# Kernel optimization log

Hardware: AMD Instinct MI355X
Metric: run time of the kernel (lower is better)

The kernel has to match this reference:

```python
import jax, jax.numpy as jnp
from jax import lax
import numpy as np

B, L, N = 128, 16, 20000
H_IN, H, H_T = 512, 1024, 128


def setup_inputs() -> dict:
    key = jax.random.key(0)
    ks = jax.random.split(key, 8)
    def xav(k, shape):
        fan_in, fan_out = shape[1], shape[0]
        a = jnp.sqrt(6.0 / (fan_in + fan_out))
        return jax.random.uniform(k, shape, jnp.float32, -a, a)
    v = jax.random.uniform(ks[0], (B, L, N), jnp.float32)
    t = jax.random.uniform(ks[1], (B, L), jnp.float32)
    W_down = xav(ks[2], (H_IN, N))
    Wt_up_w = xav(ks[3], (H_T, 1))
    Wt_up_b = jnp.zeros((H_T,), jnp.float32)
    W_vt = xav(ks[4], (H_IN, H_IN + H_T))
    k_lstm = 1.0 / jnp.sqrt(H)
    W_ih = jax.random.uniform(ks[5], (4 * H, H_IN), jnp.float32, -k_lstm, k_lstm)
    W_hh = jax.random.uniform(ks[6], (4 * H, H), jnp.float32, -k_lstm, k_lstm)
    b_ih = jnp.zeros((4 * H,), jnp.float32)
    b_hh = jnp.zeros((4 * H,), jnp.float32)
    lin_w = xav(ks[7], (1, H))
    lin_b = jnp.zeros((1,), jnp.float32)
    return {"v": v, "t": t, "W_down": W_down, "Wt_up_w": Wt_up_w,
            "Wt_up_b": Wt_up_b, "W_vt": W_vt, "W_ih": W_ih, "W_hh": W_hh,
            "b_ih": b_ih, "b_hh": b_hh, "lin_w": lin_w, "lin_b": lin_b}


def reference(v, t, W_down, Wt_up_w, Wt_up_b, W_vt, W_ih, W_hh, b_ih, b_hh, lin_w, lin_b):
    b, rw_len, n = v.shape
    h_dim = W_hh.shape[1]
    # W_down: [B,L,N] @ [N,H_in] -> [B,L,H_in]
    vd = jnp.einsum('bln,dn->bld', v, W_down)
    # Wt_up: scalar time -> [B,L,H_t]
    te = t[..., None] * Wt_up_w[:, 0] + Wt_up_b
    vt = jnp.concatenate([vd, te], axis=-1)          # [B,L,H_in+H_t]
    inputs = jnp.einsum('blk,ik->bli', vt, W_vt)     # [B,L,H_in]
    # precompute input-side LSTM gate projections for all steps
    xg = jnp.einsum('bli,gi->blg', inputs, W_ih) + b_ih  # [B,L,4H]
    xg = jnp.swapaxes(xg, 0, 1)                      # [L,B,4H] for scan

    def step(carry, xg_t):
        h, c = carry
        gates = xg_t + h @ W_hh.T + b_hh             # [B,4H]
        i, f, g, o = jnp.split(gates, 4, axis=-1)    # PyTorch gate order i,f,g,o
        i = jax.nn.sigmoid(i)
        f = jax.nn.sigmoid(f)
        g = jnp.tanh(g)
        o = jax.nn.sigmoid(o)
        c = f * c + i * g
        h = o * jnp.tanh(c)
        return (h, c), None

    h0 = jnp.zeros((b, h_dim), v.dtype)
    c0 = jnp.zeros((b, h_dim), v.dtype)
    (h, _), _ = lax.scan(step, (h0, c0), xg)
    pred = h @ lin_w.T + lin_b                       # [B,1]
    return pred
```

## Files before the change

### kernel.cpp

```cpp
#include <hip/hip_runtime.h>

typedef _Float16 f16;
typedef _Float16 f16x2 __attribute__((ext_vector_type(2)));
typedef _Float16 f16x4 __attribute__((ext_vector_type(4)));
typedef _Float16 f16x8 __attribute__((ext_vector_type(8)));
typedef float f32x4 __attribute__((ext_vector_type(4)));

__device__ __forceinline__ f32x4 mfma16(f16x8 a, f16x8 b, f32x4 c) {
  return __builtin_amdgcn_mfma_f32_16x16x32_f16(a, b, c, 0, 0, 0);
}

__device__ __forceinline__ float sigmoid_(float x) { return 1.f / (1.f + __expf(-x)); }
__device__ __forceinline__ float tanh_(float x) { return 1.f - 2.f / (__expf(2.f * x) + 1.f); }

__global__ void cvt3_kernel(const float* __restrict__ s0, f16* __restrict__ d0, int n0,
                            const float* __restrict__ s1, f16* __restrict__ d1, int n1,
                            const float* __restrict__ s2, f16* __restrict__ d2, int n2) {
  int i = blockIdx.x * 256 + threadIdx.x;
  const float* s;
  f16* d;
  int j;
  if (i < n0) {
    s = s0; d = d0; j = i;
  } else if (i < n0 + n1) {
    s = s1; d = d1; j = i - n0;
  } else if (i < n0 + n1 + n2) {
    s = s2; d = d2; j = i - n0 - n1;
  } else {
    return;
  }
  float4 v = ((const float4*)s)[j];
  f16x4 h = {(f16)v.x, (f16)v.y, (f16)v.z, (f16)v.w};
  ((f16x4*)d)[j] = h;
}

__global__ __launch_bounds__(256, 3) void gemm1_kernel(
    const float* __restrict__ A, const float* __restrict__ B, f16* __restrict__ P) {
  constexpr int K = 20000;
  __shared__ f16 Al[128][44];
  __shared__ f16 Bl[128][44];
  int tid = threadIdx.x;
  int split = blockIdx.x;
  int m0 = (blockIdx.y >> 2) * 128, n0 = (blockIdx.y & 3) * 128;
  int it0 = (split * 625) >> 4, it1 = ((split + 1) * 625) >> 4;
  int wid = tid >> 6, lane = tid & 63;
  int wm = wid & 1, wn = wid >> 1;
  int lm = lane & 15, quad = lane >> 4;
  int srow = tid >> 1, sseg = (tid & 1) * 16;

  const float* aptr = A + (size_t)(m0 + srow) * K + sseg;
  const float* bptr = B + (size_t)(n0 + srow) * K + sseg;

  float4 Ar[4], Br[4];
  {
    int k0 = it0 * 32;
#pragma unroll
    for (int j = 0; j < 4; ++j) {
      Ar[j] = *(const float4*)(aptr + k0 + j * 4);
      Br[j] = *(const float4*)(bptr + k0 + j * 4);
    }
  }

  f32x4 acc[4][4];
#pragma unroll
  for (int i = 0; i < 4; ++i)
#pragma unroll
    for (int j = 0; j < 4; ++j) acc[i][j] = (f32x4){0.f, 0.f, 0.f, 0.f};

  for (int it = it0; it < it1; ++it) {
    __syncthreads();
    {
      f16x8 pa0 = {(f16)Ar[0].x, (f16)Ar[0].y, (f16)Ar[0].z, (f16)Ar[0].w,
                   (f16)Ar[1].x, (f16)Ar[1].y, (f16)Ar[1].z, (f16)Ar[1].w};
      f16x8 pa1 = {(f16)Ar[2].x, (f16)Ar[2].y, (f16)Ar[2].z, (f16)Ar[2].w,
                   (f16)Ar[3].x, (f16)Ar[3].y, (f16)Ar[3].z, (f16)Ar[3].w};
      f16x8 pb0 = {(f16)Br[0].x, (f16)Br[0].y, (f16)Br[0].z, (f16)Br[0].w,
                   (f16)Br[1].x, (f16)Br[1].y, (f16)Br[1].z, (f16)Br[1].w};
      f16x8 pb1 = {(f16)Br[2].x, (f16)Br[2].y, (f16)Br[2].z, (f16)Br[2].w,
                   (f16)Br[3].x, (f16)Br[3].y, (f16)Br[3].z, (f16)Br[3].w};
      *(f16x8*)&Al[srow][sseg] = pa0;
      *(f16x8*)&Al[srow][sseg + 8] = pa1;
      *(f16x8*)&Bl[srow][sseg] = pb0;
      *(f16x8*)&Bl[srow][sseg + 8] = pb1;
    }
    if (it + 1 < it1) {
      int kn = (it + 1) * 32;
#pragma unroll
      for (int j = 0; j < 4; ++j) {
        Ar[j] = *(const float4*)(aptr + kn + j * 4);
        Br[j] = *(const float4*)(bptr + kn + j * 4);
      }
    }
    __syncthreads();
    f16x8 af[4];
#pragma unroll
    for (int mi = 0; mi < 4; ++mi) af[mi] = *(const f16x8*)&Al[wm * 64 + mi * 16 + lm][quad * 8];
#pragma unroll
    for (int ni = 0; ni < 4; ++ni) {
      f16x8 bf = *(const f16x8*)&Bl[wn * 64 + ni * 16 + lm][quad * 8];
#pragma unroll
      for (int mi = 0; mi < 4; ++mi) acc[mi][ni] = mfma16(af[mi], bf, acc[mi][ni]);
    }
  }
  size_t base = (size_t)split * 2048;
#pragma unroll
  for (int mi = 0; mi < 4; ++mi)
#pragma unroll
    for (int ni = 0; ni < 4; ++ni)
#pragma unroll
      for (int r = 0; r < 4; ++r) {
        int row = m0 + wm * 64 + mi * 16 + quad * 4 + r;
        int col = n0 + wn * 64 + ni * 16 + lm;
        P[(base + row) * 512 + col] = (f16)acc[mi][ni][r];
      }
}

__global__ void build_vt_kernel(const f16* __restrict__ P, const float* __restrict__ t,
                                const float* __restrict__ wtw, const float* __restrict__ wtb,
                                f16* __restrict__ vt) {
  int m = blockIdx.x;
  float tv = t[m];
  for (int c = threadIdx.x; c < 640; c += 256) {
    float val;
    if (c < 512) {
      val = 0.f;
#pragma unroll
      for (int s = 0; s < 16; ++s) val += (float)P[((size_t)s * 2048 + m) * 512 + c];
    } else {
      val = tv * wtw[c - 512] + wtb[c - 512];
    }
    vt[(size_t)m * 640 + c] = (f16)val;
  }
}

template <int TM, int TN, int EPI>
__global__ __launch_bounds__(256, 4) void gemmT_kernel(
    const f16* __restrict__ A, const f16* __restrict__ B, f16* __restrict__ out,
    const float* __restrict__ bias0, const float* __restrict__ bias1, int K_iters, int K,
    int N) {
  constexpr int FM = TM / 32, FN = TN / 32;
  __shared__ f16 Al[TM][40];
  __shared__ f16 Bl[TN][40];
  int tid = threadIdx.x;
  int m0 = blockIdx.y * TM, n0 = blockIdx.x * TN;
  int wid = tid >> 6, lane = tid & 63;
  int wm = wid & 1, wn = wid >> 1;
  int lm = lane & 15, quad = lane >> 4;

  f32x4 acc[FM][FN];
#pragma unroll
  for (int i = 0; i < FM; ++i)
#pragma unroll
    for (int j = 0; j < FN; ++j) acc[i][j] = (f32x4){0.f, 0.f, 0.f, 0.f};

  for (int it = 0; it < K_iters; ++it) {
    int k0 = it * 32;
    __syncthreads();
#pragma unroll
    for (int r = 0; r < TM / 64; ++r) {
      int slot = r * 256 + tid;
      int row = slot >> 2, seg = slot & 3;
      *(f16x8*)&Al[row][seg * 8] = *(const f16x8*)(A + (size_t)(m0 + row) * K + k0 + seg * 8);
    }
#pragma unroll
    for (int r = 0; r < TN / 64; ++r) {
      int slot = r * 256 + tid;
      int row = slot >> 2, seg = slot & 3;
      *(f16x8*)&Bl[row][seg * 8] = *(const f16x8*)(B + (size_t)(n0 + row) * K + k0 + seg * 8);
    }
    __syncthreads();
    f16x8 af[FM];
#pragma unroll
    for (int mi = 0; mi < FM; ++mi)
      af[mi] = *(const f16x8*)&Al[wm * (TM / 2) + mi * 16 + lm][quad * 8];
#pragma unroll
    for (int ni = 0; ni < FN; ++ni) {
      f16x8 bf = *(const f16x8*)&Bl[wn * (TN / 2) + ni * 16 + lm][quad * 8];
#pragma unroll
      for (int mi = 0; mi < FM; ++mi) acc[mi][ni] = mfma16(af[mi], bf, acc[mi][ni]);
    }
  }
#pragma unroll
  for (int mi = 0; mi < FM; ++mi)
#pragma unroll
    for (int ni = 0; ni < FN; ++ni)
#pragma unroll
      for (int r = 0; r < 4; ++r) {
        int row = m0 + wm * (TM / 2) + mi * 16 + quad * 4 + r;
        int col = n0 + wn * (TN / 2) + ni * 16 + lm;
        float val = acc[mi][ni][r];
        if (EPI == 0) {
          out[(size_t)row * N + col] = (f16)val;
        } else {
          int l = row & 15, b = row >> 4;
          out[(size_t)(l * 128 + b) * N + col] = (f16)(val + bias0[col] + bias1[col]);
        }
      }
}

__global__ __launch_bounds__(256, 1) void lstm_step2_kernel(
    const f16* __restrict__ h_in, const f16* __restrict__ Whh,
    const f16* __restrict__ xg_l, float* __restrict__ cT, f16* __restrict__ h_out) {
  __shared__ f16 Alf[32 * 1032];
  __shared__ float gl[4][32][17];
  __shared__ f16 hx[32][18];
  int tid = threadIdx.x;
  int w = tid >> 6, lane = tid & 63;
  int lm = lane & 15, quad = lane >> 4;
  int h0 = blockIdx.x * 16;
  int b0 = blockIdx.y * 32;

#pragma unroll
  for (int i = 0; i < 16; ++i) {
    int idx = i * 256 + tid;
    int r = idx >> 7, c8 = (idx & 127) * 8;
    *(f16x8*)&Alf[r * 1032 + c8] = *(const f16x8*)(h_in + (size_t)(b0 + r) * 1024 + c8);
  }
  const f16* wrow = Whh + ((size_t)(w << 10) + h0 + lm) * 1024 + quad * 8;
  f16x8 Bv[8];
#pragma unroll
  for (int j = 0; j < 8; ++j) Bv[j] = *(const f16x8*)(wrow + j * 32);
  f32x4 acc0 = {0.f, 0.f, 0.f, 0.f}, acc1 = {0.f, 0.f, 0.f, 0.f};
  __syncthreads();
#pragma unroll
  for (int it = 0; it < 32; ++it) {
    f16x8 bfr = Bv[it & 7];
    if (it < 24) Bv[it & 7] = *(const f16x8*)(wrow + (it + 8) * 32);
    f16x8 a0 = *(const f16x8*)&Alf[lm * 1032 + it * 32 + quad * 8];
    f16x8 a1 = *(const f16x8*)&Alf[(16 + lm) * 1032 + it * 32 + quad * 8];
    acc0 = mfma16(a0, bfr, acc0);
    acc1 = mfma16(a1, bfr, acc1);
  }
#pragma unroll
  for (int r = 0; r < 4; ++r) {
    gl[w][quad * 4 + r][lm] = acc0[r];
    gl[w][16 + quad * 4 + r][lm] = acc1[r];
  }
  __syncthreads();
#pragma unroll
  for (int half = 0; half < 2; ++half) {
    int b = tid & 31, hl = (tid >> 5) + half * 8;
    int gb = b0 + b, gh = h0 + hl;
    const f16* xr = xg_l + (size_t)gb * 4096 + gh;
    float gi = (float)xr[0] + gl[0][b][hl];
    float gf = (float)xr[1024] + gl[1][b][hl];
    float gg = (float)xr[2048] + gl[2][b][hl];
    float go = (float)xr[3072] + gl[3][b][hl];
    float iv = sigmoid_(gi), fv = sigmoid_(gf), gv = tanh_(gg), ov = sigmoid_(go);
    size_t ci = (size_t)gh * 128 + gb;
    float cc = fv * cT[ci] + iv * gv;
    cT[ci] = cc;
    hx[b][hl] = (f16)(ov * tanh_(cc));
  }
  __syncthreads();
  {
    int b = tid >> 3, e = (tid & 7) * 2;
    f16x2 hv = {hx[b][e], hx[b][e + 1]};
    *(f16x2*)(h_out + (size_t)(b0 + b) * 1024 + h0 + e) = hv;
  }
}

__global__ void pred_kernel(const f16* __restrict__ h, const float* __restrict__ w,
                            const float* __restrict__ b, float* __restrict__ out) {
  int bb = blockIdx.x, tid = threadIdx.x;
  f16x4 hv = *(const f16x4*)(h + (size_t)bb * 1024 + tid * 4);
  float4 wv = *(const float4*)(w + tid * 4);
  float s = (float)hv[0] * wv.x + (float)hv[1] * wv.y + (float)hv[2] * wv.z + (float)hv[3] * wv.w;
#pragma unroll
  for (int off = 32; off > 0; off >>= 1) s += __shfl_down(s, off);
  __shared__ float red[4];
  if ((tid & 63) == 0) red[tid >> 6] = s;
  __syncthreads();
  if (tid == 0) out[bb] = red[0] + red[1] + red[2] + red[3] + b[0];
}

extern "C" void kernel_launch(void* const* d_in, const int* in_sizes, int n_in,
                              void* d_out, int out_size, void* d_ws, size_t ws_size,
                              hipStream_t stream) {
  (void)in_sizes; (void)n_in; (void)out_size; (void)ws_size;
  const float* v      = (const float*)d_in[0];
  const float* t      = (const float*)d_in[1];
  const float* W_down = (const float*)d_in[2];
  const float* Wt_w   = (const float*)d_in[3];
  const float* Wt_b   = (const float*)d_in[4];
  const float* W_vt   = (const float*)d_in[5];
  const float* W_ih   = (const float*)d_in[6];
  const float* W_hh   = (const float*)d_in[7];
  const float* b_ih   = (const float*)d_in[8];
  const float* b_hh   = (const float*)d_in[9];
  const float* lin_w  = (const float*)d_in[10];
  const float* lin_b  = (const float*)d_in[11];

  char* ws = (char*)d_ws;
  constexpr size_t OFF_WVT = 0;
  constexpr size_t OFF_WIH = 655360;
  constexpr size_t OFF_WHH = 4849664;
  constexpr size_t OFF_VT  = 13238272;
  constexpr size_t OFF_IN  = 15859712;
  constexpr size_t OFF_P   = 17956864;
  constexpr size_t OFF_H0  = 51511296;
  constexpr size_t OFF_C   = 51773440;
  constexpr size_t OFF_H1  = 52297728;

  f16* wvt16  = (f16*)(ws + OFF_WVT);
  f16* wih16  = (f16*)(ws + OFF_WIH);
  f16* whh16  = (f16*)(ws + OFF_WHH);
  f16* vt16   = (f16*)(ws + OFF_VT);
  f16* in16   = (f16*)(ws + OFF_IN);
  f16* pxg    = (f16*)(ws + OFF_P);
  float* cT   = (float*)(ws + OFF_C);
  f16* hb[2]  = {(f16*)(ws + OFF_H0), (f16*)(ws + OFF_H1)};

  hipMemsetAsync(ws + OFF_H0, 0, 786432, stream);

  cvt3_kernel<<<6465, 256, 0, stream>>>(W_vt, wvt16, 81920, W_ih, wih16, 524288, W_hh, whh16,
                                        1048576);

  gemm1_kernel<<<dim3(16, 64), 256, 0, stream>>>(v, W_down, pxg);
  build_vt_kernel<<<2048, 256, 0, stream>>>(pxg, t, Wt_w, Wt_b, vt16);
  gemmT_kernel<64, 64, 0><<<dim3(8, 32), 256, 0, stream>>>(vt16, wvt16, in16, nullptr, nullptr,
                                                           20, 640, 512);
  gemmT_kernel<64, 128, 1><<<dim3(32, 32), 256, 0, stream>>>(in16, wih16, pxg, b_ih, b_hh, 16,
                                                             512, 4096);

  for (int s = 0; s < 16; ++s) {
    lstm_step2_kernel<<<dim3(64, 4), 256, 0, stream>>>(
        hb[s & 1], whh16, pxg + (size_t)s * 128 * 4096, cT, hb[(s + 1) & 1]);
  }
  pred_kernel<<<128, 256, 0, stream>>>(hb[0], lin_w, lin_b, (float*)d_out);
}
```

Baseline: 554.8 us.

## Fuse LSTM steps into persistent kernel with grid barrier and retile gemm1

Replaces the 16 per-step LSTM launches with one persistent kernel of 256 blocks. Each block keeps its W_hh slice resident in LDS and its cell state in registers, and steps are separated by an atomic grid barrier. The xg projection output is written in a block-friendly interleaved layout so each thread can load its gates with one vector load. gemm1 moves to 128x256 tiles with W_down pre-converted to fp16 when the workspace is large enough. This removes launch overhead and the per-step reloads of weights and cell state, but the barrier assumes all 256 blocks are co-resident.

```diff
diff --git a/kernel.cpp b/kernel.cpp
--- a/kernel.cpp
+++ b/kernel.cpp
@@ -1,4 +1,5 @@
 #include <hip/hip_runtime.h>
+#include <type_traits>
 
 typedef _Float16 f16;
 typedef _Float16 f16x2 __attribute__((ext_vector_type(2)));
@@ -12,6 +13,15 @@
 
 __device__ __forceinline__ float sigmoid_(float x) { return 1.f / (1.f + __expf(-x)); }
 __device__ __forceinline__ float tanh_(float x) { return 1.f - 2.f / (__expf(2.f * x) + 1.f); }
+
+__global__ void cvt_kernel(const float* __restrict__ src, f16* __restrict__ dst, int n4) {
+  int i = blockIdx.x * 256 + threadIdx.x;
+  if (i < n4) {
+    float4 v = ((const float4*)src)[i];
+    f16x4 h = {(f16)v.x, (f16)v.y, (f16)v.z, (f16)v.w};
+    ((f16x4*)dst)[i] = h;
+  }
+}
 
 __global__ void cvt3_kernel(const float* __restrict__ s0, f16* __restrict__ d0, int n0,
                             const float* __restrict__ s1, f16* __restrict__ d1, int n1,
@@ -34,38 +44,42 @@
   ((f16x4*)d)[j] = h;
 }
 
-__global__ __launch_bounds__(256, 3) void gemm1_kernel(
-    const float* __restrict__ A, const float* __restrict__ B, f16* __restrict__ P) {
+template <typename BT>
+__global__ __launch_bounds__(256, 2) void gemm1_kernel(
+    const float* __restrict__ A, const BT* __restrict__ B, f16* __restrict__ P) {
+  constexpr bool BF32 = std::is_same<BT, float>::value;
   constexpr int K = 20000;
-  __shared__ f16 Al[128][44];
-  __shared__ f16 Bl[128][44];
-  int tid = threadIdx.x;
-  int split = blockIdx.x;
-  int m0 = (blockIdx.y >> 2) * 128, n0 = (blockIdx.y & 3) * 128;
-  int it0 = (split * 625) >> 4, it1 = ((split + 1) * 625) >> 4;
-  int wid = tid >> 6, lane = tid & 63;
-  int wm = wid & 1, wn = wid >> 1;
-  int lm = lane & 15, quad = lane >> 4;
-  int srow = tid >> 1, sseg = (tid & 1) * 16;
-
-  const float* aptr = A + (size_t)(m0 + srow) * K + sseg;
-  const float* bptr = B + (size_t)(n0 + srow) * K + sseg;
-
-  float4 Ar[4], Br[4];
+  __shared__ f16 Al[128][40];
+  __shared__ f16 Bl[256][40];
+  const int tid = threadIdx.x;
+  const int split = blockIdx.x;
+  const int m0 = (int)(blockIdx.y >> 1) * 128, n0 = (int)(blockIdx.y & 1) * 256;
+  const int it0 = (split * 625) >> 4, it1 = ((split + 1) * 625) >> 4;
+  const int wid = tid >> 6, lane = tid & 63;
+  const int wm = wid & 1, wn = wid >> 1;
+  const int lm = lane & 15, quad = lane >> 4;
+  const int arow = tid >> 1, aseg = (tid & 1) * 16;
+
+  const float* aptr = A + (size_t)(m0 + arow) * K + aseg;
+  const BT* bptr = B + (size_t)(n0 + tid) * K;
+
+  using BReg = typename std::conditional<BF32, float4, f16x8>::type;
+  constexpr int NB = BF32 ? 8 : 4;
+  float4 Ar[4];
+  BReg Br[NB];
   {
     int k0 = it0 * 32;
 #pragma unroll
-    for (int j = 0; j < 4; ++j) {
-      Ar[j] = *(const float4*)(aptr + k0 + j * 4);
-      Br[j] = *(const float4*)(bptr + k0 + j * 4);
-    }
-  }
-
-  f32x4 acc[4][4];
+    for (int j = 0; j < 4; ++j) Ar[j] = *(const float4*)(aptr + k0 + j * 4);
+#pragma unroll
+    for (int j = 0; j < NB; ++j) Br[j] = ((const BReg*)(bptr + k0))[j];
+  }
+
+  f32x4 acc[4][8];
 #pragma unroll
   for (int i = 0; i < 4; ++i)
 #pragma unroll
-    for (int j = 0; j < 4; ++j) acc[i][j] = (f32x4){0.f, 0.f, 0.f, 0.f};
+    for (int j = 0; j < 8; ++j) acc[i][j] = (f32x4){0.f, 0.f, 0.f, 0.f};
 
   for (int it = it0; it < it1; ++it) {
     __syncthreads();
@@ -74,30 +88,35 @@
                    (f16)Ar[1].x, (f16)Ar[1].y, (f16)Ar[1].z, (f16)Ar[1].w};
       f16x8 pa1 = {(f16)Ar[2].x, (f16)Ar[2].y, (f16)Ar[2].z, (f16)Ar[2].w,
                    (f16)Ar[3].x, (f16)Ar[3].y, (f16)Ar[3].z, (f16)Ar[3].w};
-      f16x8 pb0 = {(f16)Br[0].x, (f16)Br[0].y, (f16)Br[0].z, (f16)Br[0].w,
-                   (f16)Br[1].x, (f16)Br[1].y, (f16)Br[1].z, (f16)Br[1].w};
-      f16x8 pb1 = {(f16)Br[2].x, (f16)Br[2].y, (f16)Br[2].z, (f16)Br[2].w,
-                   (f16)Br[3].x, (f16)Br[3].y, (f16)Br[3].z, (f16)Br[3].w};
-      *(f16x8*)&Al[srow][sseg] = pa0;
-      *(f16x8*)&Al[srow][sseg + 8] = pa1;
-      *(f16x8*)&Bl[srow][sseg] = pb0;
-      *(f16x8*)&Bl[srow][sseg + 8] = pb1;
+      *(f16x8*)&Al[arow][aseg] = pa0;
+      *(f16x8*)&Al[arow][aseg + 8] = pa1;
+      if constexpr (BF32) {
+#pragma unroll
+        for (int j = 0; j < 4; ++j) {
+          float4 lo = Br[2 * j], hi = Br[2 * j + 1];
+          f16x8 pb = {(f16)lo.x, (f16)lo.y, (f16)lo.z, (f16)lo.w,
+                      (f16)hi.x, (f16)hi.y, (f16)hi.z, (f16)hi.w};
+          *(f16x8*)&Bl[tid][j * 8] = pb;
+        }
+      } else {
+#pragma unroll
+        for (int j = 0; j < 4; ++j) *(f16x8*)&Bl[tid][j * 8] = Br[j];
+      }
     }
     if (it + 1 < it1) {
       int kn = (it + 1) * 32;
 #pragma unroll
-      for (int j = 0; j < 4; ++j) {
-        Ar[j] = *(const float4*)(aptr + kn + j * 4);
-        Br[j] = *(const float4*)(bptr + kn + j * 4);
-      }
+      for (int j = 0; j < 4; ++j) Ar[j] = *(const float4*)(aptr + kn + j * 4);
+#pragma unroll
+      for (int j = 0; j < NB; ++j) Br[j] = ((const BReg*)(bptr + kn))[j];
     }
     __syncthreads();
     f16x8 af[4];
 #pragma unroll
     for (int mi = 0; mi < 4; ++mi) af[mi] = *(const f16x8*)&Al[wm * 64 + mi * 16 + lm][quad * 8];
 #pragma unroll
-    for (int ni = 0; ni < 4; ++ni) {
-      f16x8 bf = *(const f16x8*)&Bl[wn * 64 + ni * 16 + lm][quad * 8];
+    for (int ni = 0; ni < 8; ++ni) {
+      f16x8 bf = *(const f16x8*)&Bl[wn * 128 + ni * 16 + lm][quad * 8];
 #pragma unroll
       for (int mi = 0; mi < 4; ++mi) acc[mi][ni] = mfma16(af[mi], bf, acc[mi][ni]);
     }
@@ -106,11 +125,11 @@
 #pragma unroll
   for (int mi = 0; mi < 4; ++mi)
 #pragma unroll
-    for (int ni = 0; ni < 4; ++ni)
+    for (int ni = 0; ni < 8; ++ni)
 #pragma unroll
       for (int r = 0; r < 4; ++r) {
         int row = m0 + wm * 64 + mi * 16 + quad * 4 + r;
-        int col = n0 + wn * 64 + ni * 16 + lm;
+        int col = n0 + wn * 128 + ni * 16 + lm;
         P[(base + row) * 512 + col] = (f16)acc[mi][ni][r];
       }
 }
@@ -193,70 +212,91 @@
           out[(size_t)row * N + col] = (f16)val;
         } else {
           int l = row & 15, b = row >> 4;
-          out[(size_t)(l * 128 + b) * N + col] = (f16)(val + bias0[col] + bias1[col]);
+          int g = col >> 10, h = col & 1023;
+          int bid = (h >> 4) * 4 + (b >> 5);
+          int t2 = ((h & 15) >> 1) * 32 + (b & 31);
+          size_t off = ((((size_t)l * 256 + bid) * 256 + t2) << 3) + g * 2 + (h & 1);
+          out[off] = (f16)(val + bias0[col] + bias1[col]);
         }
       }
 }
 
-__global__ __launch_bounds__(256, 1) void lstm_step2_kernel(
-    const f16* __restrict__ h_in, const f16* __restrict__ Whh,
-    const f16* __restrict__ xg_l, float* __restrict__ cT, f16* __restrict__ h_out) {
-  __shared__ f16 Alf[32 * 1032];
+__global__ __launch_bounds__(256, 1) void lstm_persist_kernel(
+    const f16* __restrict__ Whh, const f16* __restrict__ xg, f16* __restrict__ B0,
+    f16* __restrict__ B1, unsigned* __restrict__ bar) {
+  __shared__ f16 Wl[64 * 1032];
   __shared__ float gl[4][32][17];
-  __shared__ f16 hx[32][18];
-  int tid = threadIdx.x;
-  int w = tid >> 6, lane = tid & 63;
-  int lm = lane & 15, quad = lane >> 4;
-  int h0 = blockIdx.x * 16;
-  int b0 = blockIdx.y * 32;
-
-#pragma unroll
-  for (int i = 0; i < 16; ++i) {
-    int idx = i * 256 + tid;
-    int r = idx >> 7, c8 = (idx & 127) * 8;
-    *(f16x8*)&Alf[r * 1032 + c8] = *(const f16x8*)(h_in + (size_t)(b0 + r) * 1024 + c8);
-  }
-  const f16* wrow = Whh + ((size_t)(w << 10) + h0 + lm) * 1024 + quad * 8;
-  f16x8 Bv[8];
-#pragma unroll
-  for (int j = 0; j < 8; ++j) Bv[j] = *(const f16x8*)(wrow + j * 32);
-  f32x4 acc0 = {0.f, 0.f, 0.f, 0.f}, acc1 = {0.f, 0.f, 0.f, 0.f};
+  const int tid = threadIdx.x;
+  const int w = tid >> 6, lane = tid & 63;
+  const int lm = lane & 15, quad = lane >> 4;
+  const int bid = blockIdx.x;
+  const int h0 = (bid >> 2) * 16, b0 = (bid & 3) * 32;
+
+  for (int i = tid; i < 8192; i += 256) {
+    int r = i >> 7, c8 = (i & 127) * 8;
+    *(f16x8*)&Wl[r * 1032 + c8] =
+        *(const f16x8*)(Whh + ((size_t)((r >> 4) << 10) + h0 + (r & 15)) * 1024 + c8);
+  }
+  float c0 = 0.f, c1 = 0.f;
+  const int bl = tid & 31, h2 = tid >> 5;
+  const f16* xbase = xg + ((size_t)bid * 256 + tid) * 8;
   __syncthreads();
-#pragma unroll
-  for (int it = 0; it < 32; ++it) {
-    f16x8 bfr = Bv[it & 7];
-    if (it < 24) Bv[it & 7] = *(const f16x8*)(wrow + (it + 8) * 32);
-    f16x8 a0 = *(const f16x8*)&Alf[lm * 1032 + it * 32 + quad * 8];
-    f16x8 a1 = *(const f16x8*)&Alf[(16 + lm) * 1032 + it * 32 + quad * 8];
-    acc0 = mfma16(a0, bfr, acc0);
-    acc1 = mfma16(a1, bfr, acc1);
-  }
-#pragma unroll
-  for (int r = 0; r < 4; ++r) {
-    gl[w][quad * 4 + r][lm] = acc0[r];
-    gl[w][16 + quad * 4 + r][lm] = acc1[r];
-  }
-  __syncthreads();
-#pragma unroll
-  for (int half = 0; half < 2; ++half) {
-    int b = tid & 31, hl = (tid >> 5) + half * 8;
-    int gb = b0 + b, gh = h0 + hl;
-    const f16* xr = xg_l + (size_t)gb * 4096 + gh;
-    float gi = (float)xr[0] + gl[0][b][hl];
-    float gf = (float)xr[1024] + gl[1][b][hl];
-    float gg = (float)xr[2048] + gl[2][b][hl];
-    float go = (float)xr[3072] + gl[3][b][hl];
-    float iv = sigmoid_(gi), fv = sigmoid_(gf), gv = tanh_(gg), ov = sigmoid_(go);
-    size_t ci = (size_t)gh * 128 + gb;
-    float cc = fv * cT[ci] + iv * gv;
-    cT[ci] = cc;
-    hx[b][hl] = (f16)(ov * tanh_(cc));
-  }
-  __syncthreads();
-  {
-    int b = tid >> 3, e = (tid & 7) * 2;
-    f16x2 hv = {hx[b][e], hx[b][e + 1]};
-    *(f16x2*)(h_out + (size_t)(b0 + b) * 1024 + h0 + e) = hv;
+
+  for (int s = 0; s < 16; ++s) {
+    f16x8 xv = *(const f16x8*)(xbase + (size_t)s * 524288);
+    f32x4 acc0 = {0.f, 0.f, 0.f, 0.f}, acc1 = {0.f, 0.f, 0.f, 0.f};
+    if (s > 0) {
+      const f16* hcur = (s & 1) ? B0 : B1;
+      const f16* hr0 = hcur + (size_t)(b0 + lm) * 1024 + quad * 8;
+      const f16* hr1 = hcur + (size_t)(b0 + 16 + lm) * 1024 + quad * 8;
+      f16x8 ha0[32], ha1[32];
+#pragma unroll
+      for (int it = 0; it < 32; ++it) {
+        ha0[it] = *(const f16x8*)(hr0 + it * 32);
+        ha1[it] = *(const f16x8*)(hr1 + it * 32);
+      }
+      const f16* wb = &Wl[(w * 16 + lm) * 1032 + quad * 8];
+#pragma unroll
+      for (int it = 0; it < 32; ++it) {
+        f16x8 bfr = *(const f16x8*)(wb + it * 32);
+        acc0 = mfma16(ha0[it], bfr, acc0);
+        acc1 = mfma16(ha1[it], bfr, acc1);
+      }
+    }
+#pragma unroll
+    for (int r = 0; r < 4; ++r) {
+      gl[w][quad * 4 + r][lm] = acc0[r];
+      gl[w][16 + quad * 4 + r][lm] = acc1[r];
+    }
+    __syncthreads();
+    float hh[2];
+#pragma unroll
+    for (int j = 0; j < 2; ++j) {
+      int hl = h2 * 2 + j;
+      float gi = (float)xv[j] + gl[0][bl][hl];
+      float gf = (float)xv[2 + j] + gl[1][bl][hl];
+      float gg = (float)xv[4 + j] + gl[2][bl][hl];
+      float go = (float)xv[6 + j] + gl[3][bl][hl];
+      float iv = sigmoid_(gi), fv = sigmoid_(gf), gv = tanh_(gg), ov = sigmoid_(go);
+      float& cc = j ? c1 : c0;
+      cc = fv * cc + iv * gv;
+      hh[j] = ov * tanh_(cc);
+    }
+    f16* hnxt = (s & 1) ? B1 : B0;
+    f16x2 hv = {(f16)hh[0], (f16)hh[1]};
+    *(f16x2*)(hnxt + (size_t)(b0 + bl) * 1024 + h0 + h2 * 2) = hv;
+    if (s < 15) {
+      __syncthreads();
+      if (tid == 0) {
+        __threadfence();
+        __hip_atomic_fetch_add(bar + s * 16, 1u, __ATOMIC_RELAXED, __HIP_MEMORY_SCOPE_AGENT);
+        while (__hip_atomic_load(bar + s * 16, __ATOMIC_RELAXED, __HIP_MEMORY_SCOPE_AGENT) <
+               256u)
+          __builtin_amdgcn_s_sleep(2);
+        __threadfence();
+      }
+      __syncthreads();
+    }
   }
 }
 
@@ -277,7 +317,7 @@
 extern "C" void kernel_launch(void* const* d_in, const int* in_sizes, int n_in,
                               void* d_out, int out_size, void* d_ws, size_t ws_size,
                               hipStream_t stream) {
-  (void)in_sizes; (void)n_in; (void)out_size; (void)ws_size;
+  (void)in_sizes; (void)n_in; (void)out_size;
   const float* v      = (const float*)d_in[0];
   const float* t      = (const float*)d_in[1];
   const float* W_down = (const float*)d_in[2];
@@ -295,37 +335,47 @@
   constexpr size_t OFF_WVT = 0;
   constexpr size_t OFF_WIH = 655360;
   constexpr size_t OFF_WHH = 4849664;
-  constexpr size_t OFF_VT  = 13238272;
-  constexpr size_t OFF_IN  = 15859712;
-  constexpr size_t OFF_P   = 17956864;
-  constexpr size_t OFF_H0  = 51511296;
-  constexpr size_t OFF_C   = 51773440;
-  constexpr size_t OFF_H1  = 52297728;
-
+  constexpr size_t A_WDOWN = 13238272;
+  constexpr size_t A_VT  = 33718272;
+  constexpr size_t A_IN  = 36339712;
+  constexpr size_t A_P   = 38436864;
+  constexpr size_t A_H0  = 71991296;
+  constexpr size_t A_H1  = 72253440;
+  constexpr size_t A_BAR = 72515584;
+  constexpr size_t B_VT  = 13238272;
+  constexpr size_t B_IN  = 15859712;
+  constexpr size_t B_P   = 17956864;
+  constexpr size_t B_H0  = 51511296;
+  constexpr size_t B_H1  = 51773440;
+  constexpr size_t B_BAR = 52035584;
+
+  const bool big = ws_size >= 72516608ull;
   f16* wvt16  = (f16*)(ws + OFF_WVT);
   f16* wih16  = (f16*)(ws + OFF_WIH);
   f16* whh16  = (f16*)(ws + OFF_WHH);
-  f16* vt16   = (f16*)(ws + OFF_VT);
-  f16* in16   = (f16*)(ws + OFF_IN);
-  f16* pxg    = (f16*)(ws + OFF_P);
-  float* cT   = (float*)(ws + OFF_C);
-  f16* hb[2]  = {(f16*)(ws + OFF_H0), (f16*)(ws + OFF_H1)};
-
-  hipMemsetAsync(ws + OFF_H0, 0, 786432, stream);
-
-  cvt3_kernel<<<6465, 256, 0, stream>>>(W_vt, wvt16, 81920, W_ih, wih16, 524288, W_hh, whh16,
+  f16* vt16   = (f16*)(ws + (big ? A_VT : B_VT));
+  f16* in16   = (f16*)(ws + (big ? A_IN : B_IN));
+  f16* pxg    = (f16*)(ws + (big ? A_P : B_P));
+  f16* hb0    = (f16*)(ws + (big ? A_H0 : B_H0));
+  f16* hb1    = (f16*)(ws + (big ? A_H1 : B_H1));
+  unsigned* bar = (unsigned*)(ws + (big ? A_BAR : B_BAR));
+
+  hipMemsetAsync(bar, 0, 1024, stream);
+
+  cvt3_kernel<<<6464, 256, 0, stream>>>(W_vt, wvt16, 81920, W_ih, wih16, 524288, W_hh, whh16,
                                         1048576);
-
-  gemm1_kernel<<<dim3(16, 64), 256, 0, stream>>>(v, W_down, pxg);
+  if (big) {
+    f16* wdown16 = (f16*)(ws + A_WDOWN);
+    cvt_kernel<<<10000, 256, 0, stream>>>(W_down, wdown16, 2560000);
+    gemm1_kernel<f16><<<dim3(16, 32), 256, 0, stream>>>(v, wdown16, pxg);
+  } else {
+    gemm1_kernel<float><<<dim3(16, 32), 256, 0, stream>>>(v, W_down, pxg);
+  }
   build_vt_kernel<<<2048, 256, 0, stream>>>(pxg, t, Wt_w, Wt_b, vt16);
   gemmT_kernel<64, 64, 0><<<dim3(8, 32), 256, 0, stream>>>(vt16, wvt16, in16, nullptr, nullptr,
                                                            20, 640, 512);
   gemmT_kernel<64, 128, 1><<<dim3(32, 32), 256, 0, stream>>>(in16, wih16, pxg, b_ih, b_hh, 16,
                                                              512, 4096);
-
-  for (int s = 0; s < 16; ++s) {
-    lstm_step2_kernel<<<dim3(64, 4), 256, 0, stream>>>(
-        hb[s & 1], whh16, pxg + (size_t)s * 128 * 4096, cT, hb[(s + 1) & 1]);
-  }
-  pred_kernel<<<128, 256, 0, stream>>>(hb[0], lin_w, lin_b, (float*)d_out);
-}
+  lstm_persist_kernel<<<256, 256, 0, stream>>>(whh16, pxg, hb0, hb1, bar);
+  pred_kernel<<<128, 256, 0, stream>>>(hb1, lin_w, lin_b, (float*)d_out);
+}
```

After: 867.5 us. 1.56x slower.
